# Kernel optimization log

Hardware: AMD Instinct MI355X
Metric: run time of the kernel (lower is better)

Reference implementation:

```python
import jax, jax.numpy as jnp
import numpy as np

NUM_GROUPS = 32
EPS = 1e-5


def group_norm(x, gamma, beta):
    # x: [B, C, H, W]
    B, C, H, W = x.shape
    xg = x.reshape(B, NUM_GROUPS, C // NUM_GROUPS, H, W)
    mean = jnp.mean(xg, axis=(2, 3, 4), keepdims=True)
    var = jnp.var(xg, axis=(2, 3, 4), keepdims=True)
    xn = ((xg - mean) * jax.lax.rsqrt(var + EPS)).reshape(B, C, H, W)
    return xn * gamma[None, :, None, None] + beta[None, :, None, None]


def setup_inputs() -> dict:
    key = jax.random.key(0)
    ks = jax.random.split(key, 11)
    B, C, H, W = 16, 512, 48, 48
    scale = 1.0 / np.sqrt(C)
    return {
        "x": jax.random.normal(ks[0], (B, C, H, W), dtype=jnp.float32),
        "gn_gamma": jnp.ones((C,), dtype=jnp.float32),
        "gn_beta": jnp.zeros((C,), dtype=jnp.float32),
        "wq": jax.random.normal(ks[1], (C, C), dtype=jnp.float32) * scale,
        "bq": jnp.zeros((C,), dtype=jnp.float32),
        "wk": jax.random.normal(ks[2], (C, C), dtype=jnp.float32) * scale,
        "bk": jnp.zeros((C,), dtype=jnp.float32),
        "wv": jax.random.normal(ks[3], (C, C), dtype=jnp.float32) * scale,
        "bv": jnp.zeros((C,), dtype=jnp.float32),
        "wo": jax.random.normal(ks[4], (C, C), dtype=jnp.float32) * scale,
        "bo": jnp.zeros((C,), dtype=jnp.float32),
    }


def reference(x, gn_gamma, gn_beta, wq, bq, wk, bk, wv, bv, wo, bo):
    B, C, H, W = x.shape
    y = group_norm(x, gn_gamma, gn_beta)
    yf = y.reshape(B, C, H * W)  # [B, C, N]
    # 1x1 convs == per-position channel GEMMs
    q = jnp.einsum('oc,bcn->bon', wq, yf) + bq[None, :, None]
    k = jnp.einsum('oc,bcn->bon', wk, yf) + bk[None, :, None]
    v = jnp.einsum('oc,bcn->bon', wv, yf) + bv[None, :, None]
    # attn[b,i,j] = q[:, :, i] . k[:, :, j], scaled by sqrt(C)
    attn = jnp.einsum('bci,bcj->bij', q, k) / jnp.sqrt(jnp.float32(C))
    attn = jax.nn.softmax(attn, axis=-1)
    # out[b,c,i] = sum_j v[b,c,j] * attn[b,i,j]
    out = jnp.einsum('bcj,bij->bci', v, attn)
    out = jnp.einsum('oc,bcn->bon', wo, out) + bo[None, :, None]
    return out.reshape(B, C, H, W) + x
```

## Files before the change

### kernel.cpp

```cpp
#include <hip/hip_runtime.h>

#define DI __device__ __forceinline__

typedef __attribute__((ext_vector_type(8))) short bf16x8;
typedef __attribute__((ext_vector_type(4))) short s16x4;
typedef __attribute__((ext_vector_type(4))) float f32x4;

DI short f2bf(float f) {
  unsigned u = __builtin_bit_cast(unsigned, f);
  u += 0x7FFFu + ((u >> 16) & 1u);
  return (short)(u >> 16);
}

#define WAITVM(N) asm volatile("s_waitcnt vmcnt(" #N ")" ::: "memory")
#define AS1 __attribute__((address_space(1)))
#define AS3 __attribute__((address_space(3)))


__global__ __launch_bounds__(256) void prep_k(
    const float* __restrict__ wq, const float* __restrict__ wk,
    const float* __restrict__ wv, const float* __restrict__ wo,
    short* __restrict__ Wv, short* __restrict__ Wo,
    short* __restrict__ WkT, short* __restrict__ WqT) {
  const int i = blockIdx.x * 256 + threadIdx.x;
  const float sc = 0.04419417382415922f;
  const int o = i >> 9, c = i & 511;
  Wv[(o >> 7) * 65536 + (c >> 5) * 4096 + (o & 127) * 32 + (c & 31)] = f2bf(wv[i]);
  const int cp = (c & ~63) | ((c & 15) << 2) | ((c >> 4) & 3);
  Wo[(o >> 7) * 65536 + (cp >> 5) * 4096 + (o & 127) * 32 + (cp & 31)] = f2bf(wo[i]);
  const int tr = c * 512 + o;
  WkT[tr] = f2bf(wk[i] * sc);
  WqT[tr] = f2bf(wq[i]);
}

__global__ __launch_bounds__(256) void g0_k(const float* __restrict__ wk,
                                            const float* __restrict__ bq,
                                            float* __restrict__ g0) {
  const int c = blockIdx.x * 256 + threadIdx.x;
  float acc = 0.f;
#pragma unroll 8
  for (int o = 0; o < 512; ++o) acc += wk[o * 512 + c] * bq[o];
  g0[c] = acc * 0.04419417382415922f;
}

__global__ __launch_bounds__(256) void gn_stats(const float* __restrict__ x,
                                                float2* __restrict__ stats) {
  const int bg = blockIdx.x;
  const float4* xg = (const float4*)(x + (size_t)bg * 36864);
  float s = 0.f, q = 0.f;
  for (int i = threadIdx.x; i < 9216; i += 256) {
    float4 v = xg[i];
    s += v.x + v.y + v.z + v.w;
    q += v.x * v.x + v.y * v.y + v.z * v.z + v.w * v.w;
  }
#pragma unroll
  for (int d = 1; d < 64; d <<= 1) { s += __shfl_xor(s, d); q += __shfl_xor(q, d); }
  __shared__ float rs[4], rq[4];
  const int w = threadIdx.x >> 6;
  if ((threadIdx.x & 63) == 0) { rs[w] = s; rq[w] = q; }
  __syncthreads();
  if (threadIdx.x == 0) {
    float S = rs[0] + rs[1] + rs[2] + rs[3];
    float Q = rq[0] + rq[1] + rq[2] + rq[3];
    float mean = S * (1.f / 36864.f);
    float var  = Q * (1.f / 36864.f) - mean * mean;
    float2 o; o.x = mean; o.y = rsqrtf(var + 1e-5f);
    stats[bg] = o;
  }
}

__global__ __launch_bounds__(256) void gn_norm_t(
    const float* __restrict__ x, const float2* __restrict__ stats,
    const float* __restrict__ gamma, const float* __restrict__ beta,
    short* __restrict__ yT) {
  __shared__ float ts[64][68];
  const int n0 = blockIdx.x * 64, c0 = blockIdx.y * 64, b = blockIdx.z;
  const int t = threadIdx.x;
  {
    const int cw = t >> 4;
    const int n4 = (t & 15) * 4;
    const float* xb = x + ((size_t)b * 512 + c0) * 2304 + n0;
#pragma unroll
    for (int r4 = 0; r4 < 4; ++r4) {
      const int c = cw + r4 * 16;
      float4 v = *(const float4*)(xb + (size_t)c * 2304 + n4);
      *(float4*)&ts[c][n4] = v;
    }
  }
  __syncthreads();
  {
    const int c4 = t & 15;
    const int nw = t >> 4;
    const int cg = c0 + c4 * 4;
    const float2 ms = stats[b * 32 + (cg >> 4)];
    const float4 gm = *(const float4*)(gamma + cg);
    const float4 bt = *(const float4*)(beta + cg);
    const float a0 = ms.y * gm.x, a1 = ms.y * gm.y, a2 = ms.y * gm.z, a3 = ms.y * gm.w;
    const float d0 = bt.x - ms.x * a0, d1 = bt.y - ms.x * a1,
                d2 = bt.z - ms.x * a2, d3 = bt.w - ms.x * a3;
#pragma unroll
    for (int it = 0; it < 4; ++it) {
      const int no = nw + it * 16;
      const int n = n0 + no;
      const float v0 = ts[c4 * 4 + 0][no], v1 = ts[c4 * 4 + 1][no];
      const float v2 = ts[c4 * 4 + 2][no], v3 = ts[c4 * 4 + 3][no];
      s16x4 o = { f2bf(v0 * a0 + d0), f2bf(v1 * a1 + d1),
                  f2bf(v2 * a2 + d2), f2bf(v3 * a3 + d3) };
      *(s16x4*)(yT + (size_t)b * 2304 * 512 + (n >> 7) * 65536 +
                (cg >> 5) * 4096 + (n & 127) * 32 + (cg & 31)) = o;
    }
  }
}

template <int EPI, bool BIASROW, bool AT, bool BT, bool DT, int LDA, int LDB,
          int KSTEPS>
__global__ __launch_bounds__(256) void gemm_k(
    const short* __restrict__ A, size_t sA,
    const short* __restrict__ Bt, size_t sB,
    void* __restrict__ Dp, size_t sD,
    const float* __restrict__ bias, const float* __restrict__ resid,
    int N, int tilesM, int boff) {
  __shared__ short As[3][128 * 32];
  __shared__ short Bs[3][128 * 32];
  int bx, cb;
  if (gridDim.y == 16) {
    const int gx = gridDim.x;
    const int id = blockIdx.y * gx + blockIdx.x;
    const int xcd = id & 7, r = id >> 3;
    cb = xcd * 2 + (r >= gx ? 1 : 0);
    bx = (r >= gx) ? r - gx : r;
  } else {
    bx = blockIdx.x;
    bx = (bx & 7) * (int)(gridDim.x >> 3) + (bx >> 3);
    cb = blockIdx.y;
  }
  const int ba = cb, bb = cb + boff;
  const int tm = bx % tilesM, tn = bx / tilesM;
  const int row0 = tm * 128, col0 = tn * 128;
  const int tid = threadIdx.x, lane = tid & 63, w = tid >> 6;
  const int lr = lane & 15, lg = lane >> 4;
  const short* Ab = A + (size_t)ba * sA;
  const short* Bb = Bt + (size_t)bb * sB;
  f32x4 acc[4][4];
  const f32x4 zero = {0.f, 0.f, 0.f, 0.f};
#pragma unroll
  for (int i = 0; i < 4; ++i)
#pragma unroll
    for (int j = 0; j < 4; ++j) acc[i][j] = zero;
  const int wrow = (w & 1) * 64, wcol = (w >> 1) * 64;
  const int sw = (lg ^ ((lr >> 1) & 3)) * 8;

#define GK_STAGE(KS, BUF)                                                      \
  {                                                                            \
    _Pragma("unroll")                                                          \
    for (int j = 0; j < 2; ++j) {                                              \
      const int g = (w * 2 + j) * 64 + lane;                                   \
      const int sub8 = ((g & 3) ^ ((g >> 3) & 3)) * 8;                         \
      const short* ga = AT ? (Ab + (size_t)row0 * 512 + (KS) * 4096 +          \
                              (g >> 2) * 32 + sub8)                            \
                           : (Ab + (size_t)(row0 + (g >> 2)) * LDA +           \
                              (KS) * 32 + sub8);                               \
      const short* gb = BT ? (Bb + (size_t)col0 * 512 + (KS) * 4096 +          \
                              (g >> 2) * 32 + sub8)                            \
                           : (Bb + (size_t)(col0 + (g >> 2)) * LDB +           \
                              (KS) * 32 + sub8);                               \
      __builtin_amdgcn_global_load_lds(                                        \
          (AS1 void*)ga, (AS3 void*)&As[BUF][(w * 2 + j) * 512], 16, 0, 0);    \
      __builtin_amdgcn_global_load_lds(                                        \
          (AS1 void*)gb, (AS3 void*)&Bs[BUF][(w * 2 + j) * 512], 16, 0, 0);    \
    }                                                                          \
  }

  GK_STAGE(0, 0);
  GK_STAGE(1, 1);
  GK_STAGE(2, 2);
  int cur = 0;
  for (int ks = 0; ks < KSTEPS; ++ks) {
    if (ks + 2 < KSTEPS)      WAITVM(8);
    else if (ks + 1 < KSTEPS) WAITVM(4);
    else                      WAITVM(0);
    __builtin_amdgcn_sched_barrier(0);
    __builtin_amdgcn_s_barrier();
    bf16x8 af[4], bfr[4];
#pragma unroll
    for (int mi = 0; mi < 4; ++mi)
      af[mi] = *(const bf16x8*)&As[cur][(wrow + mi * 16 + lr) * 32 + sw];
#pragma unroll
    for (int nj = 0; nj < 4; ++nj)
      bfr[nj] = *(const bf16x8*)&Bs[cur][(wcol + nj * 16 + lr) * 32 + sw];
    __builtin_amdgcn_s_setprio(1);
#pragma unroll
    for (int mi = 0; mi < 4; ++mi)
#pragma unroll
      for (int nj = 0; nj < 4; ++nj)
        acc[mi][nj] = __builtin_amdgcn_mfma_f32_16x16x32_bf16(af[mi], bfr[nj], acc[mi][nj], 0, 0, 0);
    __builtin_amdgcn_s_setprio(0);
    __builtin_amdgcn_s_barrier();
    if (ks + 3 < KSTEPS) { GK_STAGE(ks + 3, cur) }
    cur = (cur == 2) ? 0 : cur + 1;
  }
#undef GK_STAGE

  const size_t bD = (size_t)bb * sD;
  if (EPI == 3) {
    const int colpos = col0 + wcol + lr * 4;
    const int jb = colpos >> 5, j5 = colpos & 31;
#pragma unroll
    for (int mi = 0; mi < 4; ++mi) {
#pragma unroll
      for (int r = 0; r < 4; ++r) {
        const int row = row0 + wrow + mi * 16 + lg * 4 + r;
        const float bv = bias[row];
        const int off = (jb * 32 + (row >> 4)) * 512 + ((row & 15) << 5) + j5;
        s16x4 o = { f2bf(acc[mi][0][r] + bv), f2bf(acc[mi][1][r] + bv),
                    f2bf(acc[mi][2][r] + bv), f2bf(acc[mi][3][r] + bv) };
        *(s16x4*)&((short*)Dp)[bD + off] = o;
      }
    }
  } else {
#pragma unroll
    for (int mi = 0; mi < 4; ++mi) {
#pragma unroll
      for (int nj = 0; nj < 4; ++nj) {
        const int col = col0 + wcol + nj * 16 + lr;
#pragma unroll
        for (int r = 0; r < 4; ++r) {
          const int row = row0 + wrow + mi * 16 + lg * 4 + r;
          float v = acc[mi][nj][r];
          if (EPI != 2) v += (BIASROW ? bias[row] : bias[col]);
          if (EPI == 1) {
            const size_t idx = bD + (size_t)row * N + col;
            ((float*)Dp)[idx] = v + resid[idx];
          } else {
            const size_t idx = bD + (DT
                ? (size_t)((row >> 7) * 65536 + (col >> 5) * 4096 +
                           (row & 127) * 32 + (col & 31))
                : (size_t)row * N + col);
            ((short*)Dp)[idx] = f2bf(v);
          }
        }
      }
    }
  }
}

__global__ __launch_bounds__(512, 4) void gemm_s(
    const short* __restrict__ z, const short* __restrict__ yT,
    short* __restrict__ Praw, float* __restrict__ Tsum, int b0) {
  __shared__ short As[3][128 * 32];
  __shared__ short Bs[3][256 * 32];
  int tm, tn, cb;
  if (gridDim.y == 16) {
    const int id = blockIdx.y * 162 + blockIdx.x;
    const int xcd = id & 7, r = id >> 3;
    cb = xcd * 2 + (r >= 162 ? 1 : 0);
    const int rr = (r >= 162) ? r - 162 : r;
    tm = rr % 18; tn = rr / 18;
  } else {
    cb = blockIdx.y; tm = blockIdx.x % 18; tn = blockIdx.x / 18;
  }
  const int b = b0 + cb;
  const int row0 = tm * 128, col0 = tn * 256;
  const int tid = threadIdx.x, lane = tid & 63, w = tid >> 6;
  const int lr = lane & 15, lg = lane >> 4;
  const short* Ab = z + (size_t)b * 2304 * 512;
  const short* Bb = yT + (size_t)b * 2304 * 512;
  f32x4 acc[4][4];
  const f32x4 zero = {0.f, 0.f, 0.f, 0.f};
#pragma unroll
  for (int i = 0; i < 4; ++i)
#pragma unroll
    for (int j = 0; j < 4; ++j) acc[i][j] = zero;
  const int wrow = (w & 1) * 64, wcol = (w >> 1) * 64;
  const int sw = (lg ^ ((lr >> 1) & 3)) * 8;

#define GS_STAGE(KS, BUF)                                                      \
  {                                                                            \
    const int sub8 = ((tid & 3) ^ ((tid >> 3) & 3)) * 8;                       \
    const short* ga = Ab + (size_t)row0 * 512 + (KS) * 4096 +                  \
                      (tid >> 2) * 32 + sub8;                                  \
    __builtin_amdgcn_global_load_lds(                                          \
        (AS1 void*)ga, (AS3 void*)&As[BUF][w * 512], 16, 0, 0);                \
    const short* gb0 = Bb + (size_t)col0 * 512 + (KS) * 4096 +                 \
                       (tid >> 2) * 32 + sub8;                                 \
    __builtin_amdgcn_global_load_lds(                                          \
        (AS1 void*)gb0, (AS3 void*)&Bs[BUF][w * 512], 16, 0, 0);               \
    const short* gb1 = Bb + (size_t)col0 * 512 + 65536 + (KS) * 4096 +         \
                       (tid >> 2) * 32 + sub8;                                 \
    __builtin_amdgcn_global_load_lds(                                          \
        (AS1 void*)gb1, (AS3 void*)&Bs[BUF][4096 + w * 512], 16, 0, 0);        \
  }

  GS_STAGE(0, 0);
  GS_STAGE(1, 1);
  GS_STAGE(2, 2);
  int cur = 0;
  for (int ks = 0; ks < 16; ++ks) {
    if (ks < 14)      WAITVM(6);
    else if (ks < 15) WAITVM(3);
    else              WAITVM(0);
    __builtin_amdgcn_sched_barrier(0);
    __builtin_amdgcn_s_barrier();
    bf16x8 af[4], bfr[4];
#pragma unroll
    for (int mi = 0; mi < 4; ++mi)
      af[mi] = *(const bf16x8*)&As[cur][(wrow + mi * 16 + lr) * 32 + sw];
#pragma unroll
    for (int nj = 0; nj < 4; ++nj)
      bfr[nj] = *(const bf16x8*)&Bs[cur][(wcol + nj * 16 + lr) * 32 + sw];
    __builtin_amdgcn_s_setprio(1);
#pragma unroll
    for (int mi = 0; mi < 4; ++mi)
#pragma unroll
      for (int nj = 0; nj < 4; ++nj)
        acc[mi][nj] = __builtin_amdgcn_mfma_f32_16x16x32_bf16(af[mi], bfr[nj], acc[mi][nj], 0, 0, 0);
    __builtin_amdgcn_s_setprio(0);
    __builtin_amdgcn_s_barrier();
    if (ks + 3 < 16) { GS_STAGE(ks + 3, cur) }
    cur = (cur == 2) ? 0 : cur + 1;
  }
#undef GS_STAGE
  const int tn128 = tn * 2 + (wcol >> 7);
  const int c64 = wcol & 64;
  short* Pp = Praw + ((size_t)(cb * 18 + tn128) * 2304 + row0) * 128 + c64;
  float* Ts = Tsum + ((size_t)cb * 2304 + row0) * 36 + tn128 * 2 + (c64 >> 6);
#pragma unroll
  for (int mi = 0; mi < 4; ++mi) {
#pragma unroll
    for (int r = 0; r < 4; ++r) {
      const int row = wrow + mi * 16 + lg * 4 + r;
      float pv0 = __expf(acc[mi][0][r] - 30.f);
      float pv1 = __expf(acc[mi][1][r] - 30.f);
      float pv2 = __expf(acc[mi][2][r] - 30.f);
      float pv3 = __expf(acc[mi][3][r] - 30.f);
      float sum = pv0 + pv1 + pv2 + pv3;
#pragma unroll
      for (int d = 1; d < 16; d <<= 1) sum += __shfl_xor(sum, d);
      if (lr == 0) Ts[(size_t)row * 36] = sum;
      s16x4 o = { f2bf(pv0), f2bf(pv1), f2bf(pv2), f2bf(pv3) };
      *(s16x4*)(Pp + (size_t)row * 128 + lr * 4) = o;
    }
  }
}

__global__ __launch_bounds__(256) void sum_k(
    const float* __restrict__ Tsum, float* __restrict__ linv, int nrows) {
  const int r = blockIdx.x * 256 + threadIdx.x;
  if (r >= nrows) return;
  const float* ts = Tsum + (size_t)r * 36;
  float l = 0.f;
#pragma unroll
  for (int t = 0; t < 36; ++t) l += ts[t];
  linv[r] = 1.f / l;
}

__global__ __launch_bounds__(512) void gemm_pv(
    const short* __restrict__ Praw, const float* __restrict__ linv,
    const short* __restrict__ vsrc, short* __restrict__ Dp, int b0) {
  __shared__ short As[3][144 * 32];
  int tm, cb;
  if (gridDim.y == 16) {
    const int id = blockIdx.y * 16 + blockIdx.x;
    const int xcd = id & 7, r = id >> 3;
    cb = xcd * 2 + (r >= 16 ? 1 : 0);
    tm = r & 15;
  } else {
    cb = blockIdx.y; tm = blockIdx.x;
  }
  const int bb = b0 + cb;
  const int row0 = tm * 144;
  const int tid = threadIdx.x, lane = tid & 63, w = tid >> 6;
  const int lr = lane & 15, lg = lane >> 4;
  const short* Ab = Praw + (size_t)cb * 18 * 2304 * 128;
  const short* Bb = vsrc + (size_t)bb * 512 * 2304;
  const short* Bp0 = Bb + (w * 4 + 0) * 512 + lr * 32 + lg * 8;
  const short* Bp1 = Bb + (w * 4 + 1) * 512 + lr * 32 + lg * 8;
  const short* Bp2 = Bb + (w * 4 + 2) * 512 + lr * 32 + lg * 8;
  const short* Bp3 = Bb + (w * 4 + 3) * 512 + lr * 32 + lg * 8;
  f32x4 acc[9][4];
  const f32x4 zero = {0.f, 0.f, 0.f, 0.f};
#pragma unroll
  for (int i = 0; i < 9; ++i)
#pragma unroll
    for (int j = 0; j < 4; ++j) acc[i][j] = zero;
  const int sw = (lg ^ ((lr >> 1) & 3)) * 8;

#define PVA_STAGE(KS, BUF)                                                     \
  {                                                                            \
    const int kt = (KS) >> 2, k32 = ((KS) & 3) * 32;                           \
    {                                                                          \
      const int g = tid;                                                       \
      const short* ga = Ab + ((size_t)kt * 2304 + row0 + (g >> 2)) * 128 +     \
                        k32 + (((g & 3) ^ ((g >> 3) & 3)) * 8);                \
      __builtin_amdgcn_global_load_lds(                                        \
          (AS1 void*)ga, (AS3 void*)&As[BUF][w * 512], 16, 0, 0);              \
    }                                                                          \
    if (w == 0) {                                                              \
      const int g = 512 + tid;                                                 \
      const short* ga = Ab + ((size_t)kt * 2304 + row0 + (g >> 2)) * 128 +     \
                        k32 + (((g & 3) ^ ((g >> 3) & 3)) * 8);                \
      __builtin_amdgcn_global_load_lds(                                        \
          (AS1 void*)ga, (AS3 void*)&As[BUF][4096], 16, 0, 0);                 \
    }                                                                          \
  }

#define PV_BLOAD(KS, BR)                                                       \
  {                                                                            \
    BR[0] = *(const bf16x8*)(Bp0 + (KS) * 16384);                              \
    BR[1] = *(const bf16x8*)(Bp1 + (KS) * 16384);                              \
    BR[2] = *(const bf16x8*)(Bp2 + (KS) * 16384);                              \
    BR[3] = *(const bf16x8*)(Bp3 + (KS) * 16384);                              \
  }

#define PV_ITER(KS, BUSE, BFILL)                                               \
  {                                                                            \
    if ((KS) < 70)       { if (w == 0) WAITVM(12); else WAITVM(10); }          \
    else if ((KS) == 70) { if (w == 0) WAITVM(10); else WAITVM(8); }           \
    else                 WAITVM(4);                                            \
    __builtin_amdgcn_sched_barrier(0);                                         \
    __builtin_amdgcn_s_barrier();                                              \
    bf16x8 af[9];                                                              \
    _Pragma("unroll")                                                          \
    for (int mi = 0; mi < 9; ++mi)                                             \
      af[mi] = *(const bf16x8*)&As[cur][(mi * 16 + lr) * 32 + sw];             \
    __builtin_amdgcn_s_setprio(1);                                             \
    _Pragma("unroll")                                                          \
    for (int mi = 0; mi < 9; ++mi)                                             \
      _Pragma("unroll")                                                        \
      for (int nj = 0; nj < 4; ++nj)                                           \
        acc[mi][nj] = __builtin_amdgcn_mfma_f32_16x16x32_bf16(                 \
            af[mi], BUSE[nj], acc[mi][nj], 0, 0, 0);                           \
    __builtin_amdgcn_s_setprio(0);                                             \
    __builtin_amdgcn_s_barrier();                                              \
    if ((KS) + 2 < 72) PV_BLOAD((KS) + 2, BFILL);                              \
    if ((KS) + 3 < 72) PVA_STAGE((KS) + 3, cur);                               \
    cur = (cur == 2) ? 0 : cur + 1;                                            \
  }

  bf16x8 bA[4], bB[4];
  PVA_STAGE(0, 0);
  PVA_STAGE(1, 1);
  PVA_STAGE(2, 2);
  PV_BLOAD(0, bA);
  PV_BLOAD(1, bB);
  int cur = 0;
  for (int ks = 0; ks < 72; ks += 2) {
    PV_ITER(ks, bA, bA);
    PV_ITER(ks + 1, bB, bB);
  }
#undef PV_ITER
#undef PV_BLOAD
#undef PVA_STAGE

  const float* lv = linv + (size_t)cb * 2304 + row0;
  short* Db = Dp + (size_t)bb * 2304 * 512;
  const int col = w * 64 + lr * 4;
  const int coff = (col >> 5) * 4096 + (col & 31);
#pragma unroll
  for (int mi = 0; mi < 9; ++mi) {
#pragma unroll
    for (int r = 0; r < 4; ++r) {
      const int row = mi * 16 + lg * 4 + r;
      const float s = lv[row];
      const int R = row0 + row;
      s16x4 o = { f2bf(acc[mi][0][r] * s), f2bf(acc[mi][1][r] * s),
                  f2bf(acc[mi][2][r] * s), f2bf(acc[mi][3][r] * s) };
      *(s16x4*)(Db + (R >> 7) * 65536 + coff + (R & 127) * 32) = o;
    }
  }
}

extern "C" void kernel_launch(void* const* d_in, const int* in_sizes, int n_in,
                              void* d_out, int out_size, void* d_ws, size_t ws_size,
                              hipStream_t stream) {
  const float* x     = (const float*)d_in[0];
  const float* gamma = (const float*)d_in[1];
  const float* beta  = (const float*)d_in[2];
  const float* wq    = (const float*)d_in[3];
  const float* bq    = (const float*)d_in[4];
  const float* wk    = (const float*)d_in[5];
  const float* wv    = (const float*)d_in[7];
  const float* bv    = (const float*)d_in[8];
  const float* wo    = (const float*)d_in[9];
  const float* bo    = (const float*)d_in[10];

  char* ws = (char*)d_ws;
  float2* stats = (float2*)(ws + 0);
  short*  Wv    = (short*)(ws + 8192);
  short*  Wo    = (short*)(ws + 532480);
  short*  WkT   = (short*)(ws + 1056768);
  short*  WqT   = (short*)(ws + 1581056);
  short*  G     = (short*)(ws + 2105344);
  float*  g0    = (float*)(ws + 2629632);
  short*  yT    = (short*)(ws + 2631680);
  short*  zoT   = (short*)(ws + 40380416);
  short*  vbuf  = (short*)(ws + 78129152);
  short*  Praw  = (short*)(ws + 115877888);
  float*  out   = (float*)d_out;

  const size_t base = 115877888ull;
  const size_t per  = 10616832ull + 331776ull + 9216ull;
  int CH = 16;
  if (ws_size < base + 16 * per) CH = (ws_size >= base + 8 * per) ? 8 : 4;
  float* Tsum = (float*)(ws + base + (size_t)CH * 10616832ull);
  float* linv = (float*)(ws + base + (size_t)CH * (10616832ull + 331776ull));

  const size_t sBN = (size_t)2304 * 512;

  prep_k<<<1024, 256, 0, stream>>>(wq, wk, wv, wo, Wv, Wo, WkT, WqT);
  g0_k<<<2, 256, 0, stream>>>(wk, bq, g0);
  gn_stats<<<512, 256, 0, stream>>>(x, stats);
  gn_norm_t<<<dim3(36, 8, 16), 256, 0, stream>>>(x, stats, gamma, beta, yT);
  gemm_k<2, false, false, false, true, 512, 512, 16><<<dim3(16, 1), 256, 0, stream>>>(
      WkT, 0, WqT, 0, G, 0, nullptr, nullptr, 512, 4, 0);
  gemm_k<3, true, true, true, false, 512, 512, 16><<<dim3(72, 16), 256, 0, stream>>>(
      Wv, 0, yT, sBN, vbuf, sBN, bv, nullptr, 2304, 4, 0);
  gemm_k<0, false, true, true, true, 512, 512, 16><<<dim3(72, 16), 256, 0, stream>>>(
      yT, sBN, G, 0, zoT, sBN, g0, nullptr, 512, 18, 0);

  for (int b0 = 0; b0 < 16; b0 += CH) {
    const int n = (16 - b0 < CH) ? (16 - b0) : CH;
    gemm_s<<<dim3(162, n), 512, 0, stream>>>(zoT, yT, Praw, Tsum, b0);
    sum_k<<<(n * 2304 + 255) / 256, 256, 0, stream>>>(Tsum, linv, n * 2304);
    gemm_pv<<<dim3(16, n), 512, 0, stream>>>(Praw, linv, vbuf, zoT, b0);
  }
  gemm_k<1, true, true, true, false, 512, 512, 16><<<dim3(72, 16), 256, 0, stream>>>(
      Wo, 0, zoT, sBN, out, (size_t)512 * 2304, bo, x, 2304, 4, 0);
}
```

Before: 415.4 us.

## Use 128x256-tile 512-thread GEMM kernel for batched projection GEMMs

Adds a gemm_k2 kernel with 8 waves and a 128x256 output tile, and routes the V projection, the z projection and the output projection through it, halving the grid for each. Each A tile staged in LDS is now reused across twice as many output columns, which cuts global and LDS load traffic per MFMA. The original gemm_k is reduced to the unbatched, bias-free weight-product case. The cost is larger LDS use per block and fewer blocks (576 per launch) to spread across the CUs.

After: 417.3 us. About the same (+0.4%).

```diff
diff --git a/kernel.cpp b/kernel.cpp
--- a/kernel.cpp
+++ b/kernel.cpp
@@ -112,35 +112,20 @@
   }
 }
 
-template <int EPI, bool BIASROW, bool AT, bool BT, bool DT, int LDA, int LDB,
-          int KSTEPS>
+template <int EPI, bool AT, bool BT, bool DT, int KSTEPS>
 __global__ __launch_bounds__(256) void gemm_k(
-    const short* __restrict__ A, size_t sA,
-    const short* __restrict__ Bt, size_t sB,
-    void* __restrict__ Dp, size_t sD,
-    const float* __restrict__ bias, const float* __restrict__ resid,
-    int N, int tilesM, int boff) {
+    const short* __restrict__ A, const short* __restrict__ Bt,
+    void* __restrict__ Dp, int N, int tilesM) {
   __shared__ short As[3][128 * 32];
   __shared__ short Bs[3][128 * 32];
-  int bx, cb;
-  if (gridDim.y == 16) {
-    const int gx = gridDim.x;
-    const int id = blockIdx.y * gx + blockIdx.x;
-    const int xcd = id & 7, r = id >> 3;
-    cb = xcd * 2 + (r >= gx ? 1 : 0);
-    bx = (r >= gx) ? r - gx : r;
-  } else {
-    bx = blockIdx.x;
-    bx = (bx & 7) * (int)(gridDim.x >> 3) + (bx >> 3);
-    cb = blockIdx.y;
-  }
-  const int ba = cb, bb = cb + boff;
+  int bx = blockIdx.x;
+  bx = (bx & 7) * (int)(gridDim.x >> 3) + (bx >> 3);
   const int tm = bx % tilesM, tn = bx / tilesM;
   const int row0 = tm * 128, col0 = tn * 128;
   const int tid = threadIdx.x, lane = tid & 63, w = tid >> 6;
   const int lr = lane & 15, lg = lane >> 4;
-  const short* Ab = A + (size_t)ba * sA;
-  const short* Bb = Bt + (size_t)bb * sB;
+  const short* Ab = A;
+  const short* Bb = Bt;
   f32x4 acc[4][4];
   const f32x4 zero = {0.f, 0.f, 0.f, 0.f};
 #pragma unroll
@@ -158,11 +143,11 @@
       const int sub8 = ((g & 3) ^ ((g >> 3) & 3)) * 8;                         \
       const short* ga = AT ? (Ab + (size_t)row0 * 512 + (KS) * 4096 +          \
                               (g >> 2) * 32 + sub8)                            \
-                           : (Ab + (size_t)(row0 + (g >> 2)) * LDA +           \
+                           : (Ab + (size_t)(row0 + (g >> 2)) * 512 +           \
                               (KS) * 32 + sub8);                               \
       const short* gb = BT ? (Bb + (size_t)col0 * 512 + (KS) * 4096 +          \
                               (g >> 2) * 32 + sub8)                            \
-                           : (Bb + (size_t)(col0 + (g >> 2)) * LDB +           \
+                           : (Bb + (size_t)(col0 + (g >> 2)) * 512 +           \
                               (KS) * 32 + sub8);                               \
       __builtin_amdgcn_global_load_lds(                                        \
           (AS1 void*)ga, (AS3 void*)&As[BUF][(w * 2 + j) * 512], 16, 0, 0);    \
@@ -201,7 +186,105 @@
   }
 #undef GK_STAGE
 
-  const size_t bD = (size_t)bb * sD;
+#pragma unroll
+  for (int mi = 0; mi < 4; ++mi) {
+#pragma unroll
+    for (int nj = 0; nj < 4; ++nj) {
+      const int col = col0 + wcol + nj * 16 + lr;
+#pragma unroll
+      for (int r = 0; r < 4; ++r) {
+        const int row = row0 + wrow + mi * 16 + lg * 4 + r;
+        const size_t idx = DT
+            ? (size_t)((row >> 7) * 65536 + (col >> 5) * 4096 +
+                       (row & 127) * 32 + (col & 31))
+            : (size_t)row * N + col;
+        ((short*)Dp)[idx] = f2bf(acc[mi][nj][r]);
+      }
+    }
+  }
+}
+
+template <int EPI, bool BIASROW>
+__global__ __launch_bounds__(512, 4) void gemm_k2(
+    const short* __restrict__ A, size_t sA,
+    const short* __restrict__ Bt, size_t sB,
+    void* __restrict__ Dp, size_t sD,
+    const float* __restrict__ bias, const float* __restrict__ resid,
+    int N, int tilesM) {
+  __shared__ short As[3][128 * 32];
+  __shared__ short Bs[3][256 * 32];
+  int tm, tn, cb;
+  if (gridDim.y == 16) {
+    const int id = blockIdx.y * 36 + blockIdx.x;
+    const int xcd = id & 7, r = id >> 3;
+    cb = xcd * 2 + (r >= 36 ? 1 : 0);
+    const int rr = (r >= 36) ? r - 36 : r;
+    tm = rr % tilesM; tn = rr / tilesM;
+  } else {
+    cb = blockIdx.y; tm = blockIdx.x % tilesM; tn = blockIdx.x / tilesM;
+  }
+  const int row0 = tm * 128, col0 = tn * 256;
+  const int tid = threadIdx.x, lane = tid & 63, w = tid >> 6;
+  const int lr = lane & 15, lg = lane >> 4;
+  const short* Ab = A + (size_t)cb * sA;
+  const short* Bb = Bt + (size_t)cb * sB;
+  f32x4 acc[4][4];
+  const f32x4 zero = {0.f, 0.f, 0.f, 0.f};
+#pragma unroll
+  for (int i = 0; i < 4; ++i)
+#pragma unroll
+    for (int j = 0; j < 4; ++j) acc[i][j] = zero;
+  const int wrow = (w & 1) * 64, wcol = (w >> 1) * 64;
+  const int sw = (lg ^ ((lr >> 1) & 3)) * 8;
+
+#define K2_STAGE(KS, BUF)                                                      \
+  {                                                                            \
+    const int sub8 = ((tid & 3) ^ ((tid >> 3) & 3)) * 8;                       \
+    const short* ga = Ab + (size_t)row0 * 512 + (KS) * 4096 +                  \
+                      (tid >> 2) * 32 + sub8;                                  \
+    __builtin_amdgcn_global_load_lds(                                          \
+        (AS1 void*)ga, (AS3 void*)&As[BUF][w * 512], 16, 0, 0);                \
+    const short* gb0 = Bb + (size_t)col0 * 512 + (KS) * 4096 +                 \
+                       (tid >> 2) * 32 + sub8;                                 \
+    __builtin_amdgcn_global_load_lds(                                          \
+        (AS1 void*)gb0, (AS3 void*)&Bs[BUF][w * 512], 16, 0, 0);               \
+    const short* gb1 = Bb + (size_t)col0 * 512 + 65536 + (KS) * 4096 +         \
+                       (tid >> 2) * 32 + sub8;                                 \
+    __builtin_amdgcn_global_load_lds(                                          \
+        (AS1 void*)gb1, (AS3 void*)&Bs[BUF][4096 + w * 512], 16, 0, 0);        \
+  }
+
+  K2_STAGE(0, 0);
+  K2_STAGE(1, 1);
+  K2_STAGE(2, 2);
+  int cur = 0;
+  for (int ks = 0; ks < 16; ++ks) {
+    if (ks < 14)      WAITVM(6);
+    else if (ks < 15) WAITVM(3);
+    else              WAITVM(0);
+    __builtin_amdgcn_sched_barrier(0);
+    __builtin_amdgcn_s_barrier();
+    bf16x8 af[4], bfr[4];
+#pragma unroll
+    for (int mi = 0; mi < 4; ++mi)
+      af[mi] = *(const bf16x8*)&As[cur][(wrow + mi * 16 + lr) * 32 + sw];
+#pragma unroll
+    for (int nj = 0; nj < 4; ++nj)
+      bfr[nj] = *(const bf16x8*)&Bs[cur][(wcol + nj * 16 + lr) * 32 + sw];
+    __builtin_amdgcn_s_setprio(1);
+#pragma unroll
+    for (int mi = 0; mi < 4; ++mi)
+#pragma unroll
+      for (int nj = 0; nj < 4; ++nj)
+        acc[mi][nj] = __builtin_amdgcn_mfma_f32_16x16x32_bf16(af[mi], bfr[nj], acc[mi][nj], 0, 0, 0);
+    __builtin_amdgcn_s_setprio(0);
+    __builtin_amdgcn_s_barrier();
+    if (ks + 3 < 16) { K2_STAGE(ks + 3, cur) }
+    cur = (cur == 2) ? 0 : cur + 1;
+  }
+#undef K2_STAGE
+
+  const size_t bD = (size_t)cb * sD;
   if (EPI == 3) {
     const int colpos = col0 + wcol + lr * 4;
     const int jb = colpos >> 5, j5 = colpos & 31;
@@ -226,16 +309,14 @@
 #pragma unroll
         for (int r = 0; r < 4; ++r) {
           const int row = row0 + wrow + mi * 16 + lg * 4 + r;
-          float v = acc[mi][nj][r];
-          if (EPI != 2) v += (BIASROW ? bias[row] : bias[col]);
+          float v = acc[mi][nj][r] + (BIASROW ? bias[row] : bias[col]);
           if (EPI == 1) {
             const size_t idx = bD + (size_t)row * N + col;
             ((float*)Dp)[idx] = v + resid[idx];
           } else {
-            const size_t idx = bD + (DT
-                ? (size_t)((row >> 7) * 65536 + (col >> 5) * 4096 +
-                           (row & 127) * 32 + (col & 31))
-                : (size_t)row * N + col);
+            const size_t idx = bD +
+                (size_t)((row >> 7) * 65536 + (col >> 5) * 4096 +
+                         (row & 127) * 32 + (col & 31));
             ((short*)Dp)[idx] = f2bf(v);
           }
         }
@@ -511,12 +592,12 @@
   g0_k<<<2, 256, 0, stream>>>(wk, bq, g0);
   gn_stats<<<512, 256, 0, stream>>>(x, stats);
   gn_norm_t<<<dim3(36, 8, 16), 256, 0, stream>>>(x, stats, gamma, beta, yT);
-  gemm_k<2, false, false, false, true, 512, 512, 16><<<dim3(16, 1), 256, 0, stream>>>(
-      WkT, 0, WqT, 0, G, 0, nullptr, nullptr, 512, 4, 0);
-  gemm_k<3, true, true, true, false, 512, 512, 16><<<dim3(72, 16), 256, 0, stream>>>(
-      Wv, 0, yT, sBN, vbuf, sBN, bv, nullptr, 2304, 4, 0);
-  gemm_k<0, false, true, true, true, 512, 512, 16><<<dim3(72, 16), 256, 0, stream>>>(
-      yT, sBN, G, 0, zoT, sBN, g0, nullptr, 512, 18, 0);
+  gemm_k<2, false, false, true, 16><<<dim3(16, 1), 256, 0, stream>>>(
+      WkT, WqT, G, 512, 4);
+  gemm_k2<3, true><<<dim3(36, 16), 512, 0, stream>>>(
+      Wv, 0, yT, sBN, vbuf, sBN, bv, nullptr, 2304, 4);
+  gemm_k2<0, false><<<dim3(36, 16), 512, 0, stream>>>(
+      yT, sBN, G, 0, zoT, sBN, g0, nullptr, 512, 18);
 
   for (int b0 = 0; b0 < 16; b0 += CH) {
     const int n = (16 - b0 < CH) ? (16 - b0) : CH;
@@ -524,6 +605,6 @@
     sum_k<<<(n * 2304 + 255) / 256, 256, 0, stream>>>(Tsum, linv, n * 2304);
     gemm_pv<<<dim3(16, n), 512, 0, stream>>>(Praw, linv, vbuf, zoT, b0);
   }
-  gemm_k<1, true, true, true, false, 512, 512, 16><<<dim3(72, 16), 256, 0, stream>>>(
-      Wo, 0, zoT, sBN, out, (size_t)512 * 2304, bo, x, 2304, 4, 0);
-}
+  gemm_k2<1, true><<<dim3(36, 16), 512, 0, stream>>>(
+      Wo, 0, zoT, sBN, out, (size_t)512 * 2304, bo, x, 2304, 4);
+}
```
